# Kernel optimization log

Measured on AMD Instinct MI355X. Metric: run time of the kernel, lower is better.

Reference implementation:

```python
import jax, jax.numpy as jnp
import numpy as np

B, F, D_IN, H, HEADS, NC = 2048, 64, 32, 128, 4, 16
EPG = 128            # random intra-graph edges per graph
N = B * F            # 131072 nodes
E = B * EPG          # 262144 edges (self-loops added in reference, like PyG GATConv)
LRELU_ATT = 0.2      # PyG GATConv negative_slope
LRELU_CLS = 0.01     # nn.LeakyReLU default


def setup_inputs() -> dict:
    key = jax.random.key(0)
    ks = jax.random.split(key, 24)
    emb = jax.random.normal(ks[0], (B, F, D_IN), jnp.float32)
    # per-graph random connectivity, offset so graphs are disjoint
    src_l = jax.random.randint(ks[1], (B, EPG), 0, F)
    tgt_l = jax.random.randint(ks[2], (B, EPG), 0, F)
    off = (jnp.arange(B) * F)[:, None]
    edge_index = jnp.stack([(src_l + off).reshape(-1), (tgt_l + off).reshape(-1)]).astype(jnp.int32)
    batch_idx = jnp.repeat(jnp.arange(B), F).astype(jnp.int32)
    s = 0.05
    return {
        'emb': emb, 'edge_index': edge_index, 'batch_idx': batch_idx,
        # fused aligner (single unique dim 32)
        'W_align': s * jax.random.normal(ks[3], (D_IN, H), jnp.float32),
        'b_align': jnp.zeros((H,), jnp.float32),
        'gate_logits': jnp.full((F,), 2.2, jnp.float32),
        # GATConv 1: in=H, out=H per head, heads=4, concat
        'W1': s * jax.random.normal(ks[4], (H, HEADS * H), jnp.float32),
        'a_src1': s * jax.random.normal(ks[5], (HEADS, H), jnp.float32),
        'a_dst1': s * jax.random.normal(ks[6], (HEADS, H), jnp.float32),
        'b1': jnp.zeros((HEADS * H,), jnp.float32),
        # GATConv 2: in=HEADS*H, out=H, heads=1, concat=False
        'W2': s * jax.random.normal(ks[7], (HEADS * H, H), jnp.float32),
        'a_src2': s * jax.random.normal(ks[8], (1, H), jnp.float32),
        'a_dst2': s * jax.random.normal(ks[9], (1, H), jnp.float32),
        'b2': jnp.zeros((H,), jnp.float32),
        # classifier MLP
        'Wc1': s * jax.random.normal(ks[10], (H, H // 2), jnp.float32),
        'bc1': jnp.zeros((H // 2,), jnp.float32),
        'Wc2': s * jax.random.normal(ks[11], (H // 2, NC), jnp.float32),
        'bc2': jnp.zeros((NC,), jnp.float32),
    }


def gat_layer(x, src, tgt, W, a_src, a_dst, b, concat):
    heads, dout = a_src.shape
    n = x.shape[0]
    h = (x @ W).reshape(n, heads, dout)                       # [N,h,d]
    e = jax.nn.leaky_relu(jnp.einsum('nhd,hd->nh', h, a_src)[src]
                          + jnp.einsum('nhd,hd->nh', h, a_dst)[tgt], LRELU_ATT)  # [E,h]
    m = jax.ops.segment_max(e, tgt, num_segments=n)           # segment softmax over in-neighbors
    p = jnp.exp(e - m[tgt])
    ssum = jax.ops.segment_sum(p, tgt, num_segments=n)
    alpha = p / (ssum[tgt] + 1e-16)
    out = jax.ops.segment_sum(h[src] * alpha[:, :, None], tgt, num_segments=n)
    out = out.reshape(n, heads * dout) if concat else out.mean(axis=1)
    return out + b


def reference(emb, edge_index, batch_idx, W_align, b_align, gate_logits,
              W1, a_src1, a_dst1, b1, W2, a_src2, a_dst2, b2, Wc1, bc1, Wc2, bc2):
    n = emb.shape[0] * emb.shape[1]
    aligned = emb @ W_align + b_align                         # fused align: [B,F,H]
    gate = jax.nn.sigmoid(gate_logits)                        # [F]
    x = (aligned * gate[None, :, None]).reshape(n, -1)        # gated node features [N,H]
    # add self-loops (GATConv default), eval mode -> dropout is identity
    loops = jnp.arange(n, dtype=edge_index.dtype)
    src = jnp.concatenate([edge_index[0], loops])
    tgt = jnp.concatenate([edge_index[1], loops])
    x = gat_layer(x, src, tgt, W1, a_src1, a_dst1, b1, True)  # [N, 4*H]
    x = jax.nn.elu(x)
    x = gat_layer(x, src, tgt, W2, a_src2, a_dst2, b2, False) # [N, H]
    gsum = jax.ops.segment_sum(x, batch_idx, num_segments=B)  # global_mean_pool
    cnt = jax.ops.segment_sum(jnp.ones((n, 1), x.dtype), batch_idx, num_segments=B)
    g = gsum / cnt                                            # [B, H]
    hc = jax.nn.leaky_relu(g @ Wc1 + bc1, LRELU_CLS)
    logits = hc @ Wc2 + bc2                                   # [B, NC]
    return logits, gate
```

## Files before the change

kernel.cpp:

```cpp
#include <hip/hip_runtime.h>
#include <math.h>

#define BLK 256

constexpr int Bg    = 2048;
constexpr int Fn    = 64;
constexpr int DIN   = 32;
constexpr int Hd    = 128;
constexpr int HEADS = 4;
constexpr int NC    = 16;
constexpr int EPG   = 128;
constexpr int Etot  = Bg * EPG;
constexpr int W1C   = HEADS * Hd;
constexpr int NSTR  = 68;
constexpr int EROW  = 136;
constexpr int PROW  = 68;
constexpr int NE    = EPG + Fn;

typedef __attribute__((ext_vector_type(8))) __bf16 bf16x8;
typedef __attribute__((ext_vector_type(4))) __bf16 bf16x4;
typedef __attribute__((ext_vector_type(4))) float  f32x4;

__device__ __align__(16) __bf16 g_wcombT[W1C * DIN];
__device__ float g_c1[W1C];
__device__ float g_c1s[16];
__device__ __align__(16) __bf16 g_w1F[HEADS*8*64*8];
__device__ __align__(16) __bf16 g_w2F[HEADS*4*8*64*8];
__device__ __align__(16) __bf16 g_wscF[HEADS*4*64*8];
__device__ __align__(16) __bf16 g_bs1F[64*8];

__global__ __launch_bounds__(BLK) void prep1(
    const float* __restrict__ Wa, const float* __restrict__ ba,
    const float* __restrict__ W1)
{
  __shared__ float WaS[DIN * Hd];
  const int tid = threadIdx.x;
  for (int i = tid; i < DIN * Hd; i += BLK) {
    int k = i >> 7, m = i & 127;
    WaS[m * DIN + k] = Wa[i];
  }
  __syncthreads();

  int i = blockIdx.x * BLK + tid;
  if (i < DIN * W1C) {
    int k = i & 31, n = i >> 5;
    float a0 = 0.f, a1 = 0.f, a2 = 0.f, a3 = 0.f;
    #pragma unroll
    for (int m = 0; m < Hd; m += 4) {
      a0 += WaS[(m  )*DIN + k] * W1[(m  )*W1C + n];
      a1 += WaS[(m+1)*DIN + k] * W1[(m+1)*W1C + n];
      a2 += WaS[(m+2)*DIN + k] * W1[(m+2)*W1C + n];
      a3 += WaS[(m+3)*DIN + k] * W1[(m+3)*W1C + n];
    }
    g_wcombT[i] = (__bf16)(a0 + a1 + a2 + a3);
  } else if (i < DIN*W1C + W1C) {
    int n = i - DIN*W1C;
    float a0 = 0.f, a1 = 0.f, a2 = 0.f, a3 = 0.f;
    #pragma unroll
    for (int m = 0; m < Hd; m += 4) {
      a0 += ba[m  ] * W1[(m  )*W1C + n];
      a1 += ba[m+1] * W1[(m+1)*W1C + n];
      a2 += ba[m+2] * W1[(m+2)*W1C + n];
      a3 += ba[m+3] * W1[(m+3)*W1C + n];
    }
    g_c1[n] = a0 + a1 + a2 + a3;
  }
}

constexpr int R_W2F  = 65536;
constexpr int R_W1F  = 16384;
constexpr int R_WSCZ = 8192;
constexpr int R_WSCD = 4096;
constexpr int R_BS1Z = 512;
constexpr int R_BS1D = 1024;
constexpr int R_C1S  = 128;
constexpr int B0 = R_W2F;
constexpr int B1 = B0 + R_W1F;
constexpr int B2 = B1 + R_WSCZ;
constexpr int B3 = B2 + R_WSCD;
constexpr int B4 = B3 + R_BS1Z;
constexpr int B5 = B4 + R_BS1D;
constexpr int P2_TOT = B5 + R_C1S;

__global__ __launch_bounds__(BLK) void prep2(
    const float* __restrict__ W2,
    const float* __restrict__ as1, const float* __restrict__ ad1,
    const float* __restrict__ as2, const float* __restrict__ ad2)
{
  int i = blockIdx.x * BLK + threadIdx.x;
  if (i < B0) {
    int k = i >> 7, n = i & 127;
    int hh = k >> 7, Ks = (k >> 5) & 3, q = (k >> 3) & 3, j = k & 7;
    int Nt = n >> 4, l = n & 15;
    int idx = (((hh*4 + Ks)*8 + Nt)*64 + (q*16 + l))*8 + j;
    g_w2F[idx] = (__bf16)W2[i];
  } else if (i < B1) {
    int j = i - B0;
    int jj = j & 7, lane = (j >> 3) & 63, T = j >> 9;
    int hh = T >> 3, Nt = T & 7;
    int q = lane >> 4, l = lane & 15;
    g_w1F[j] = g_wcombT[(hh*Hd + Nt*16 + l)*DIN + q*8 + jj];
  } else if (i < B2) {
    int j = i - B1;
    int lane = (j >> 3) & 63, c = lane & 15;
    if (c >= 2) g_wscF[j] = (__bf16)0.f;
  } else if (i < B3) {
    int j = i - B2;
    int p = j & 3, c = (j >> 2) & 1, k = j >> 3;
    const float* av = c ? ad2 : as2;
    float a0 = 0.f, a1 = 0.f, a2 = 0.f, a3 = 0.f;
    #pragma unroll
    for (int q = 0; q < 32; q += 4) {
      int f = p*32 + q;
      a0 += W2[(size_t)k*Hd + f    ] * av[f    ];
      a1 += W2[(size_t)k*Hd + f + 1] * av[f + 1];
      a2 += W2[(size_t)k*Hd + f + 2] * av[f + 2];
      a3 += W2[(size_t)k*Hd + f + 3] * av[f + 3];
    }
    float a = a0 + a1 + a2 + a3;
    a += __shfl_xor(a, 1);
    a += __shfl_xor(a, 2);
    if (p == 0) {
      int T = k >> 5, q2 = (k >> 3) & 3, jj = k & 7;
      g_wscF[(T*64 + q2*16 + c)*8 + jj] = (__bf16)a;
    }
  } else if (i < B4) {
    int j = i - B3;
    int lane = j >> 3, c = lane & 15;
    if (c >= 8) g_bs1F[j] = (__bf16)0.f;
  } else if (i < B5) {
    int j = i - B4;
    int p = j & 3, c = (j >> 2) & 7, kk = j >> 5;
    int h = c >> 1;
    const float* av = (c & 1) ? (ad1 + h*Hd) : (as1 + h*Hd);
    float a0 = 0.f, a1 = 0.f, a2 = 0.f, a3 = 0.f;
    #pragma unroll
    for (int q = 0; q < 32; q += 4) {
      int f = p*32 + q;
      a0 += (float)g_wcombT[(h*Hd + f    )*DIN + kk] * av[f    ];
      a1 += (float)g_wcombT[(h*Hd + f + 1)*DIN + kk] * av[f + 1];
      a2 += (float)g_wcombT[(h*Hd + f + 2)*DIN + kk] * av[f + 2];
      a3 += (float)g_wcombT[(h*Hd + f + 3)*DIN + kk] * av[f + 3];
    }
    float a = a0 + a1 + a2 + a3;
    a += __shfl_xor(a, 1);
    a += __shfl_xor(a, 2);
    if (p == 0) {
      int q2 = kk >> 3, jj = kk & 7;
      g_bs1F[(q2*16 + c)*8 + jj] = (__bf16)a;
    }
  } else if (i < P2_TOT) {
    int j = i - B5;
    int p = j & 7, c = j >> 3;
    float a = 0.f;
    if (c < 8) {
      int h = c >> 1;
      const float* av = (c & 1) ? (ad1 + h*Hd) : (as1 + h*Hd);
      #pragma unroll
      for (int q = 0; q < 16; ++q) {
        int f = p*16 + q;
        a += g_c1[h*Hd + f] * av[f];
      }
    }
    a += __shfl_xor(a, 1);
    a += __shfl_xor(a, 2);
    a += __shfl_xor(a, 4);
    if (p == 0) g_c1s[c] = a;
  }
}

__global__ __launch_bounds__(BLK, 2) void gat_main(
    const float* __restrict__ emb, const int* __restrict__ ei,
    const float* __restrict__ gate_logits,
    const float* __restrict__ b1, const float* __restrict__ b2,
    const float* __restrict__ Wc1, const float* __restrict__ bc1,
    const float* __restrict__ Wc2, const float* __restrict__ bc2,
    float* __restrict__ out)
{
  __shared__ __align__(16) __bf16 hT[Hd * NSTR];
  __shared__ __align__(16) __bf16 eluS[Fn * EROW];
  __shared__ __align__(16) __bf16 Pbf[HEADS][Fn * PROW];
  __shared__ float sS1s[HEADS][Fn], sS1d[HEADS][Fn];
  __shared__ float sSum[HEADS][Fn];
  __shared__ float sSrc[Fn], sDst[Fn], gateS[Fn];
  __shared__ float gpool[Hd], hcS[Fn];
  __shared__ __align__(16) __bf16 wS[Fn];

  unsigned* cells = (unsigned*)eluS;

  const int b    = blockIdx.x;
  const int tid  = threadIdx.x;
  const int lane = tid & 63;
  const int wv   = tid >> 6;
  const int quad = lane >> 4;
  const int l15  = lane & 15;
  const int nodeBase = wv * 16;
  const int m0   = wv * 32;
  const int base = b * Fn;

  const f32x4 zero4 = {0.f, 0.f, 0.f, 0.f};

  int es = 0, et = 0, ecell = 0;
  if (tid < NE) {
    if (tid < EPG) {
      es = ei[(size_t)b*EPG + tid] - base;
      et = ei[(size_t)Etot + (size_t)b*EPG + tid] - base;
    } else {
      es = et = tid - EPG;
    }
    ecell = et * Fn + es;
  }
  #pragma unroll
  for (int i = 0; i < 16; ++i) cells[tid + i*BLK] = 0u;
  {
    float4* p4 = (float4*)&Pbf[0][0];
    const float4 z4 = {0.f,0.f,0.f,0.f};
    #pragma unroll
    for (int k = 0; k < 8; ++k) p4[tid + k*BLK] = z4;
    if (tid < 128) p4[2048 + tid] = z4;
  }
  ((float*)sSum)[tid] = 0.f;
  if (tid < Fn) {
    float g = 1.f / (1.f + expf(-gate_logits[tid]));
    gateS[tid] = g;
    if (b == 0) out[Bg*NC + tid] = g;
  }
  float4 e0, e1;
  {
    const float* ar = emb + ((size_t)base + nodeBase + l15) * DIN + quad * 8;
    e0 = *(const float4*)ar;
    e1 = *(const float4*)(ar + 4);
  }
  __syncthreads();

  bool rep = false;
  if (tid < NE) rep = (atomicAdd(&cells[ecell], 1u) == 0u);

  float gq[4];
  #pragma unroll
  for (int r = 0; r < 4; ++r) gq[r] = gateS[nodeBase + quad*4 + r];

  bf16x8 Af;
  {
    const float gl = gateS[nodeBase + l15];
    Af[0]=(__bf16)(e0.x*gl); Af[1]=(__bf16)(e0.y*gl); Af[2]=(__bf16)(e0.z*gl); Af[3]=(__bf16)(e0.w*gl);
    Af[4]=(__bf16)(e1.x*gl); Af[5]=(__bf16)(e1.y*gl); Af[6]=(__bf16)(e1.z*gl); Af[7]=(__bf16)(e1.w*gl);
  }
  {
    bf16x8 Bs = *(const bf16x8*)(g_bs1F + lane*8);
    f32x4 ds = __builtin_amdgcn_mfma_f32_16x16x32_bf16(Af, Bs, zero4, 0, 0, 0);
    if (l15 < 8) {
      const float cc = g_c1s[l15];
      const int h = l15 >> 1;
      float* dstArr = (l15 & 1) ? &sS1d[h][0] : &sS1s[h][0];
      #pragma unroll
      for (int r = 0; r < 4; ++r) {
        int m = nodeBase + quad*4 + r;
        dstArr[m] = ds[r] + gq[r] * cc;
      }
    }
  }
  #pragma unroll
  for (int Nt = 0; Nt < 8; ++Nt) {
    const int n = Nt*16 + l15;
    bf16x8 Bf = *(const bf16x8*)(g_w1F + ((0*8 + Nt)*64 + lane)*8);
    f32x4 d = __builtin_amdgcn_mfma_f32_16x16x32_bf16(Af, Bf, zero4, 0, 0, 0);
    const float c1v = g_c1[0*Hd + n];
    bf16x4 hw;
    #pragma unroll
    for (int r = 0; r < 4; ++r) hw[r] = (__bf16)(d[r] + c1v * gq[r]);
    *(bf16x4*)(hT + n*NSTR + nodeBase + quad*4) = hw;
  }
  __syncthreads();

  float fm = 0.f;
  if (tid < NE && rep) {
    fm = (float)cells[ecell];
    #pragma unroll
    for (int hh = 0; hh < HEADS; ++hh) {
      float e = sS1s[hh][es] + sS1d[hh][et];
      e = (e > 0.f) ? e : 0.2f * e;
      float pe = fm * __expf(e);
      Pbf[hh][et*PROW + es] = (__bf16)pe;
      atomicAdd(&sSum[hh][et], pe);
    }
  }
  __syncthreads();

  f32x4 acc[8];
  #pragma unroll
  for (int i = 0; i < 8; ++i) acc[i] = zero4;
  f32x4 accS = zero4;

  for (int hh = 0; hh < HEADS; ++hh) {
    {
      bf16x8 Ac[2][2];
      #pragma unroll
      for (int Mi = 0; Mi < 2; ++Mi)
        #pragma unroll
        for (int Ks = 0; Ks < 2; ++Ks)
          Ac[Mi][Ks] = *(const bf16x8*)(hT + (m0 + Mi*16 + l15)*NSTR + Ks*32 + quad*8);
      float4 b1v[2];
      #pragma unroll
      for (int Mi = 0; Mi < 2; ++Mi)
        b1v[Mi] = *(const float4*)&b1[hh*Hd + m0 + Mi*16 + quad*4];
      #pragma unroll
      for (int Nt = 0; Nt < 4; ++Nt) {
        bf16x8 B0f = *(const bf16x8*)(Pbf[hh] + (Nt*16 + l15)*PROW + quad*8);
        bf16x8 B1f = *(const bf16x8*)(Pbf[hh] + (Nt*16 + l15)*PROW + 32 + quad*8);
        const int t = Nt*16 + l15;
        const float si = 1.f / (sSum[hh][t] + 1e-16f);
        #pragma unroll
        for (int Mi = 0; Mi < 2; ++Mi) {
          f32x4 d = __builtin_amdgcn_mfma_f32_16x16x32_bf16(Ac[Mi][0], B0f, zero4, 0, 0, 0);
          d = __builtin_amdgcn_mfma_f32_16x16x32_bf16(Ac[Mi][1], B1f, d, 0, 0, 0);
          bf16x4 w;
          #pragma unroll
          for (int r = 0; r < 4; ++r) {
            float hv = d[r]*si + b1v[Mi][r];
            hv = (hv > 0.f) ? hv : (__expf(hv) - 1.f);
            w[r] = (__bf16)hv;
          }
          *(bf16x4*)(eluS + t*EROW + m0 + Mi*16 + quad*4) = w;
        }
      }
    }
    __syncthreads();

    #pragma unroll
    for (int Ks = 0; Ks < 4; ++Ks) {
      bf16x8 A2 = *(const bf16x8*)(eluS + (nodeBase + l15)*EROW + Ks*32 + quad*8);
      #pragma unroll
      for (int Nt = 0; Nt < 8; ++Nt) {
        bf16x8 B2 = *(const bf16x8*)(g_w2F + (((hh*4 + Ks)*8 + Nt)*64 + lane)*8);
        acc[Nt] = __builtin_amdgcn_mfma_f32_16x16x32_bf16(A2, B2, acc[Nt], 0, 0, 0);
      }
      bf16x8 Bs2 = *(const bf16x8*)(g_wscF + ((hh*4 + Ks)*64 + lane)*8);
      accS = __builtin_amdgcn_mfma_f32_16x16x32_bf16(A2, Bs2, accS, 0, 0, 0);
    }
    if (hh == 0) {
      float4* p4 = (float4*)&Pbf[0][0];
      const float4 z4 = {0.f,0.f,0.f,0.f};
      p4[tid] = z4; p4[tid + 256] = z4;
      if (tid < 32) p4[tid + 512] = z4;
      if (tid < Fn) sSum[0][tid] = 0.f;
    }
    if (hh < 3) {
      #pragma unroll
      for (int Nt = 0; Nt < 8; ++Nt) {
        const int n = Nt*16 + l15;
        bf16x8 Bf = *(const bf16x8*)(g_w1F + (((hh+1)*8 + Nt)*64 + lane)*8);
        f32x4 d = __builtin_amdgcn_mfma_f32_16x16x32_bf16(Af, Bf, zero4, 0, 0, 0);
        const float c1v = g_c1[(hh+1)*Hd + n];
        bf16x4 hw;
        #pragma unroll
        for (int r = 0; r < 4; ++r) hw[r] = (__bf16)(d[r] + c1v * gq[r]);
        *(bf16x4*)(hT + n*NSTR + nodeBase + quad*4) = hw;
      }
    } else {
      #pragma unroll
      for (int Nt = 0; Nt < 8; ++Nt) {
        const int n = Nt*16 + l15;
        bf16x4 hw;
        #pragma unroll
        for (int r = 0; r < 4; ++r) hw[r] = (__bf16)acc[Nt][r];
        *(bf16x4*)(hT + n*NSTR + nodeBase + quad*4) = hw;
      }
      if (l15 == 0) {
        #pragma unroll
        for (int r = 0; r < 4; ++r) sSrc[nodeBase + quad*4 + r] = accS[r];
      } else if (l15 == 1) {
        #pragma unroll
        for (int r = 0; r < 4; ++r) sDst[nodeBase + quad*4 + r] = accS[r];
      }
    }
    __syncthreads();
  }

  if (tid < NE && rep) {
    float e = sSrc[es] + sDst[et];
    e = (e > 0.f) ? e : 0.2f * e;
    float pe = fm * __expf(e);
    Pbf[0][et*PROW + es] = (__bf16)pe;
    atomicAdd(&sSum[0][et], pe);
  }
  __syncthreads();

  {
    const int s_ = tid >> 2, part = tid & 3;
    float a = 0.f;
    #pragma unroll
    for (int q = 0; q < 16; ++q) {
      const int t = part*16 + q;
      a += (1.f / (sSum[0][t] + 1e-16f)) * (float)Pbf[0][t*PROW + s_];
    }
    a += __shfl_xor(a, 1);
    a += __shfl_xor(a, 2);
    if (part == 0) wS[s_] = (__bf16)(a * (1.f/64.f));
  }
  __syncthreads();

  {
    #pragma unroll
    for (int Mi = 0; Mi < 2; ++Mi) {
      f32x4 d = zero4;
      #pragma unroll
      for (int Ks = 0; Ks < 2; ++Ks) {
        bf16x8 A = *(const bf16x8*)(hT + (m0 + Mi*16 + l15)*NSTR + Ks*32 + quad*8);
        bf16x8 Bw = *(const bf16x8*)(wS + Ks*32 + quad*8);
        d = __builtin_amdgcn_mfma_f32_16x16x32_bf16(A, Bw, d, 0, 0, 0);
      }
      if (l15 == 0) {
        #pragma unroll
        for (int r = 0; r < 4; ++r) {
          const int f = m0 + Mi*16 + quad*4 + r;
          gpool[f] = d[r] + b2[f];
        }
      }
    }
  }
  __syncthreads();

  {
    const int c = tid >> 2, p = tid & 3;
    float a = 0.f;
    #pragma unroll
    for (int i = 0; i < 32; ++i) {
      const int k = p*32 + i;
      a += gpool[k] * Wc1[k*Fn + c];
    }
    a += __shfl_xor(a, 1);
    a += __shfl_xor(a, 2);
    if (p == 0) {
      a += bc1[c];
      hcS[c] = (a > 0.f) ? a : 0.01f * a;
    }
  }
  __syncthreads();

  {
    const int c = tid >> 4, p = tid & 15;
    float a = 0.f;
    #pragma unroll
    for (int i = 0; i < 4; ++i) {
      const int k = p*4 + i;
      a += hcS[k] * Wc2[k*NC + c];
    }
    a += __shfl_xor(a, 1);
    a += __shfl_xor(a, 2);
    a += __shfl_xor(a, 4);
    a += __shfl_xor(a, 8);
    if (p == 0) out[b*NC + c] = a + bc2[c];
  }
}

extern "C" void kernel_launch(void* const* d_in, const int* in_sizes, int n_in,
                              void* d_out, int out_size, void* d_ws, size_t ws_size,
                              hipStream_t stream) {
  const float* emb = (const float*)d_in[0];
  const int*   ei  = (const int*)  d_in[1];
  const float* Wa  = (const float*)d_in[3];
  const float* ba  = (const float*)d_in[4];
  const float* gl  = (const float*)d_in[5];
  const float* W1  = (const float*)d_in[6];
  const float* as1 = (const float*)d_in[7];
  const float* ad1 = (const float*)d_in[8];
  const float* b1  = (const float*)d_in[9];
  const float* W2  = (const float*)d_in[10];
  const float* as2 = (const float*)d_in[11];
  const float* ad2 = (const float*)d_in[12];
  const float* b2  = (const float*)d_in[13];
  const float* Wc1 = (const float*)d_in[14];
  const float* bc1 = (const float*)d_in[15];
  const float* Wc2 = (const float*)d_in[16];
  const float* bc2 = (const float*)d_in[17];
  float* out = (float*)d_out;

  const int prep1N = DIN*W1C + W1C;
  hipLaunchKernelGGL(prep1, dim3((prep1N + BLK - 1)/BLK), dim3(BLK), 0, stream,
                     Wa, ba, W1);
  hipLaunchKernelGGL(prep2, dim3((P2_TOT + BLK - 1)/BLK), dim3(BLK), 0, stream,
                     W2, as1, ad1, as2, ad2);
  hipLaunchKernelGGL(gat_main, dim3(Bg), dim3(BLK), 0, stream,
                     emb, ei, gl, b1, b2, Wc1, bc1, Wc2, bc2, out);
}
```

Baseline: 209.4 us.

## Double-buffer attention matrices and alias shared buffers to fit three blocks per CU

Shrinks LDS per block by keeping only two per-head attention matrices in a ping-pong buffer, computing the next head's edge weights inside the head loop, and storing row sums in the padding columns of each attention row. Small scratch arrays (gate, src/dst scores, pool, hidden) are aliased into the eluS and Pbf regions, and EROW is reduced. The launch bound is raised to 3 blocks per CU to increase occupancy. In exchange it adds a per-head zeroing pass and edge-weight computation inside the loop, and the aliasing relies on careful ordering of lifetimes.

```diff
diff --git a/kernel.cpp b/kernel.cpp
--- a/kernel.cpp
+++ b/kernel.cpp
@@ -13,7 +13,7 @@
 constexpr int Etot  = Bg * EPG;
 constexpr int W1C   = HEADS * Hd;
 constexpr int NSTR  = 68;
-constexpr int EROW  = 136;
+constexpr int EROW  = 132;
 constexpr int PROW  = 68;
 constexpr int NE    = EPG + Fn;
 
@@ -169,7 +169,8 @@
   }
 }
 
-__global__ __launch_bounds__(BLK, 2) void gat_main(
+#define SUMP(buf, t) ((float*)((char*)&Pbf[buf][(t)*PROW] + 128))
+__global__ __launch_bounds__(BLK, 3) void gat_main(
     const float* __restrict__ emb, const int* __restrict__ ei,
     const float* __restrict__ gate_logits,
     const float* __restrict__ b1, const float* __restrict__ b2,
@@ -179,14 +180,16 @@
 {
   __shared__ __align__(16) __bf16 hT[Hd * NSTR];
   __shared__ __align__(16) __bf16 eluS[Fn * EROW];
-  __shared__ __align__(16) __bf16 Pbf[HEADS][Fn * PROW];
+  __shared__ __align__(16) __bf16 Pbf[2][Fn * PROW];
   __shared__ float sS1s[HEADS][Fn], sS1d[HEADS][Fn];
-  __shared__ float sSum[HEADS][Fn];
-  __shared__ float sSrc[Fn], sDst[Fn], gateS[Fn];
-  __shared__ float gpool[Hd], hcS[Fn];
-  __shared__ __align__(16) __bf16 wS[Fn];
 
   unsigned* cells = (unsigned*)eluS;
+  float*   gateS  = (float*)(eluS + 8192);
+  float*   sSrc   = (float*)&Pbf[1][0];
+  float*   sDst   = sSrc + Fn;
+  __bf16*  wS     = (__bf16*)(sDst + Fn);
+  float*   gpool  = (float*)(wS + Fn);
+  float*   hcS    = gpool + Hd;
 
   const int b    = blockIdx.x;
   const int tid  = threadIdx.x;
@@ -216,10 +219,9 @@
     float4* p4 = (float4*)&Pbf[0][0];
     const float4 z4 = {0.f,0.f,0.f,0.f};
     #pragma unroll
-    for (int k = 0; k < 8; ++k) p4[tid + k*BLK] = z4;
-    if (tid < 128) p4[2048 + tid] = z4;
-  }
-  ((float*)sSum)[tid] = 0.f;
+    for (int k = 0; k < 4; ++k) p4[tid + k*BLK] = z4;
+    if (tid < 64) p4[1024 + tid] = z4;
+  }
   if (tid < Fn) {
     float g = 1.f / (1.f + expf(-gate_logits[tid]));
     gateS[tid] = g;
@@ -276,14 +278,11 @@
   float fm = 0.f;
   if (tid < NE && rep) {
     fm = (float)cells[ecell];
-    #pragma unroll
-    for (int hh = 0; hh < HEADS; ++hh) {
-      float e = sS1s[hh][es] + sS1d[hh][et];
-      e = (e > 0.f) ? e : 0.2f * e;
-      float pe = fm * __expf(e);
-      Pbf[hh][et*PROW + es] = (__bf16)pe;
-      atomicAdd(&sSum[hh][et], pe);
-    }
+    float e = sS1s[0][es] + sS1d[0][et];
+    e = (e > 0.f) ? e : 0.2f * e;
+    float pe = fm * __expf(e);
+    Pbf[0][et*PROW + es] = (__bf16)pe;
+    atomicAdd(SUMP(0, et), pe);
   }
   __syncthreads();
 
@@ -293,6 +292,7 @@
   f32x4 accS = zero4;
 
   for (int hh = 0; hh < HEADS; ++hh) {
+    const int cur = hh & 1;
     {
       bf16x8 Ac[2][2];
       #pragma unroll
@@ -306,10 +306,10 @@
         b1v[Mi] = *(const float4*)&b1[hh*Hd + m0 + Mi*16 + quad*4];
       #pragma unroll
       for (int Nt = 0; Nt < 4; ++Nt) {
-        bf16x8 B0f = *(const bf16x8*)(Pbf[hh] + (Nt*16 + l15)*PROW + quad*8);
-        bf16x8 B1f = *(const bf16x8*)(Pbf[hh] + (Nt*16 + l15)*PROW + 32 + quad*8);
+        bf16x8 B0f = *(const bf16x8*)(Pbf[cur] + (Nt*16 + l15)*PROW + quad*8);
+        bf16x8 B1f = *(const bf16x8*)(Pbf[cur] + (Nt*16 + l15)*PROW + 32 + quad*8);
         const int t = Nt*16 + l15;
-        const float si = 1.f / (sSum[hh][t] + 1e-16f);
+        const float si = 1.f / (*SUMP(cur, t) + 1e-16f);
         #pragma unroll
         for (int Mi = 0; Mi < 2; ++Mi) {
           f32x4 d = __builtin_amdgcn_mfma_f32_16x16x32_bf16(Ac[Mi][0], B0f, zero4, 0, 0, 0);
@@ -325,6 +325,12 @@
         }
       }
     }
+    if (hh >= 1) {
+      float4* p4 = (float4*)&Pbf[(hh+1)&1][0];
+      const float4 z4 = {0.f,0.f,0.f,0.f};
+      p4[tid] = z4; p4[tid + 256] = z4;
+      if (tid < 32) p4[tid + 512] = z4;
+    }
     __syncthreads();
 
     #pragma unroll
@@ -337,13 +343,6 @@
       }
       bf16x8 Bs2 = *(const bf16x8*)(g_wscF + ((hh*4 + Ks)*64 + lane)*8);
       accS = __builtin_amdgcn_mfma_f32_16x16x32_bf16(A2, Bs2, accS, 0, 0, 0);
-    }
-    if (hh == 0) {
-      float4* p4 = (float4*)&Pbf[0][0];
-      const float4 z4 = {0.f,0.f,0.f,0.f};
-      p4[tid] = z4; p4[tid + 256] = z4;
-      if (tid < 32) p4[tid + 512] = z4;
-      if (tid < Fn) sSum[0][tid] = 0.f;
     }
     if (hh < 3) {
       #pragma unroll
@@ -357,6 +356,13 @@
         for (int r = 0; r < 4; ++r) hw[r] = (__bf16)(d[r] + c1v * gq[r]);
         *(bf16x4*)(hT + n*NSTR + nodeBase + quad*4) = hw;
       }
+      if (tid < NE && rep) {
+        float e = sS1s[hh+1][es] + sS1d[hh+1][et];
+        e = (e > 0.f) ? e : 0.2f * e;
+        float pe = fm * __expf(e);
+        Pbf[(hh+1)&1][et*PROW + es] = (__bf16)pe;
+        atomicAdd(SUMP((hh+1)&1, et), pe);
+      }
     } else {
       #pragma unroll
       for (int Nt = 0; Nt < 8; ++Nt) {
@@ -382,7 +388,7 @@
     e = (e > 0.f) ? e : 0.2f * e;
     float pe = fm * __expf(e);
     Pbf[0][et*PROW + es] = (__bf16)pe;
-    atomicAdd(&sSum[0][et], pe);
+    atomicAdd(SUMP(0, et), pe);
   }
   __syncthreads();
 
@@ -392,7 +398,7 @@
     #pragma unroll
     for (int q = 0; q < 16; ++q) {
       const int t = part*16 + q;
-      a += (1.f / (sSum[0][t] + 1e-16f)) * (float)Pbf[0][t*PROW + s_];
+      a += (1.f / (*SUMP(0, t) + 1e-16f)) * (float)Pbf[0][t*PROW + s_];
     }
     a += __shfl_xor(a, 1);
     a += __shfl_xor(a, 2);
@@ -453,6 +459,7 @@
     if (p == 0) out[b*NC + c] = a + bc2[c];
   }
 }
+#undef SUMP
 
 extern "C" void kernel_launch(void* const* d_in, const int* in_sizes, int n_in,
                               void* d_out, int out_size, void* d_ws, size_t ws_size,
```

After: 188.1 us. -10.2%, faster.
